# Kernel tuning notes

Hardware: AMD Instinct MI355X
Metric: run time of the kernel (lower is better)

Reference implementation:

```python
import jax, jax.numpy as jnp
import numpy as np


def setup_inputs() -> dict:
    key = jax.random.key(0)
    k1, k2 = jax.random.split(key)
    B, C, H, W = 16, 64, 144, 144
    x = jax.random.normal(k1, (B, C, H, W), dtype=jnp.float32)
    y = jax.random.normal(k2, (B, C, H, W), dtype=jnp.float32)
    return {"x": x, "y": y, "shape": 144}


def reference(x, y, shape):
    # Restrict to the [0:shape, 0:shape] spatial window the Python loop covers.
    xs = x[:, :, :shape, :shape]
    ys = y[:, :, :shape, :shape]
    # Per-pixel reductions over batch AND channel (torch .sum() reduces all
    # remaining dims of x[:, :, i, j], i.e. both B and C).
    fz = jnp.einsum('bchw,bchw->hw', xs, ys)        # [shape, shape]
    xx = jnp.einsum('bchw,bchw->hw', xs, xs)
    yy = jnp.einsum('bchw,bchw->hw', ys, ys)
    fm = jnp.sqrt(xx) * jnp.sqrt(yy)
    loss = jnp.sum(jnp.arccos(fz / fm))
    return loss / (shape ** 2)
```

## Files before the change

### kernel.cpp

```cpp
#include <hip/hip_runtime.h>
#include <math.h>


constexpr int PLANE = 144 * 144;
constexpr int QUADS = PLANE / 4;
constexpr int BC    = 16 * 64;
constexpr int QPB   = 16;
constexpr int NG    = 32;
constexpr int NBLK  = QUADS / QPB;

__device__ inline void xor_fold(float4& v, int mask) {
    v.x += __shfl_xor(v.x, mask);
    v.y += __shfl_xor(v.y, mask);
    v.z += __shfl_xor(v.z, mask);
    v.w += __shfl_xor(v.w, mask);
}

__global__ __launch_bounds__(512) void spe_partial(const float4* __restrict__ x,
                                                   const float4* __restrict__ y,
                                                   float* __restrict__ bsum)
{
    const int tid = threadIdx.x;
    const int q   = tid & (QPB - 1);
    const int g   = tid >> 4;
    const int qg  = blockIdx.x * QPB + q;

    float4 fz = make_float4(0.f, 0.f, 0.f, 0.f);
    float4 xx = make_float4(0.f, 0.f, 0.f, 0.f);
    float4 yy = make_float4(0.f, 0.f, 0.f, 0.f);

    size_t idx = (size_t)g * QUADS + (size_t)qg;
    const size_t step = (size_t)NG * QUADS;
    #pragma unroll 4
    for (int i = 0; i < BC / NG; ++i) {
        float4 a = x[idx];
        float4 b = y[idx];
        fz.x = fmaf(a.x, b.x, fz.x); fz.y = fmaf(a.y, b.y, fz.y);
        fz.z = fmaf(a.z, b.z, fz.z); fz.w = fmaf(a.w, b.w, fz.w);
        xx.x = fmaf(a.x, a.x, xx.x); xx.y = fmaf(a.y, a.y, xx.y);
        xx.z = fmaf(a.z, a.z, xx.z); xx.w = fmaf(a.w, a.w, xx.w);
        yy.x = fmaf(b.x, b.x, yy.x); yy.y = fmaf(b.y, b.y, yy.y);
        yy.z = fmaf(b.z, b.z, yy.z); yy.w = fmaf(b.w, b.w, yy.w);
        idx += step;
    }

    xor_fold(fz, 16); xor_fold(fz, 32);
    xor_fold(xx, 16); xor_fold(xx, 32);
    xor_fold(yy, 16); xor_fold(yy, 32);

    __shared__ float4 lfz[8][QPB], lxx[8][QPB], lyy[8][QPB];
    const int wave = tid >> 6;
    if ((tid & 63) < QPB) {
        lfz[wave][q] = fz; lxx[wave][q] = xx; lyy[wave][q] = yy;
    }
    __syncthreads();

    float s = 0.f;
    if (tid < QPB) {
        float4 F = lfz[0][tid], X = lxx[0][tid], Y = lyy[0][tid];
        #pragma unroll
        for (int wv = 1; wv < 8; ++wv) {
            F.x += lfz[wv][tid].x; F.y += lfz[wv][tid].y;
            F.z += lfz[wv][tid].z; F.w += lfz[wv][tid].w;
            X.x += lxx[wv][tid].x; X.y += lxx[wv][tid].y;
            X.z += lxx[wv][tid].z; X.w += lxx[wv][tid].w;
            Y.x += lyy[wv][tid].x; Y.y += lyy[wv][tid].y;
            Y.z += lyy[wv][tid].z; Y.w += lyy[wv][tid].w;
        }
        float r0 = F.x / (sqrtf(X.x) * sqrtf(Y.x));
        float r1 = F.y / (sqrtf(X.y) * sqrtf(Y.y));
        float r2 = F.z / (sqrtf(X.z) * sqrtf(Y.z));
        float r3 = F.w / (sqrtf(X.w) * sqrtf(Y.w));
        r0 = fminf(1.f, fmaxf(-1.f, r0));
        r1 = fminf(1.f, fmaxf(-1.f, r1));
        r2 = fminf(1.f, fmaxf(-1.f, r2));
        r3 = fminf(1.f, fmaxf(-1.f, r3));
        s = acosf(r0) + acosf(r1) + acosf(r2) + acosf(r3);
    }
    if (tid < 64) {
        #pragma unroll
        for (int off = 32; off >= 1; off >>= 1) s += __shfl_down(s, off);
        if (tid == 0) bsum[blockIdx.x] = s;
    }
}

__global__ __launch_bounds__(512) void spe_final(const float* __restrict__ bsum,
                                                 float* __restrict__ out)
{
    __shared__ float l[8];
    const int t = threadIdx.x;
    float s = (t < NBLK) ? bsum[t] : 0.f;
    #pragma unroll
    for (int off = 32; off >= 1; off >>= 1) s += __shfl_down(s, off);
    if ((t & 63) == 0) l[t >> 6] = s;
    __syncthreads();
    if (t == 0) {
        float tot = 0.f;
        #pragma unroll
        for (int i = 0; i < 8; ++i) tot += l[i];
        out[0] = tot * (1.0f / (float)PLANE);
    }
}

extern "C" void kernel_launch(void* const* d_in, const int* in_sizes, int n_in,
                              void* d_out, int out_size, void* d_ws, size_t ws_size,
                              hipStream_t stream) {
    const float4* x = (const float4*)d_in[0];
    const float4* y = (const float4*)d_in[1];
    float* bsum = (float*)d_ws;
    float* out  = (float*)d_out;

    spe_partial<<<NBLK, 512, 0, stream>>>(x, y, bsum);
    spe_final<<<1, 512, 0, stream>>>(bsum, out);
}
```

Baseline: 35.99 us.

## Split batch-channel reduction across grid y and add a second combine stage

The first kernel previously ran only 324 blocks, each reducing all 1024 batch-channel planes for 64 pixels. The reduction axis is now split eight ways over a second grid dimension (2592 blocks, 4 fully unrolled iterations each), and per-split partial sums are written to workspace. A new stage-2 kernel combines the splits and computes acos per pixel, and a small final kernel sums the block results. The aim is more parallelism and memory-level concurrency on a bandwidth-bound reduction, paid for with an extra launch and roughly 2 MB of partial-sum traffic.

```diff
diff --git a/kernel.cpp b/kernel.cpp
--- a/kernel.cpp
+++ b/kernel.cpp
@@ -7,7 +7,12 @@
 constexpr int BC    = 16 * 64;
 constexpr int QPB   = 16;
 constexpr int NG    = 32;
+constexpr int SPLIT = 8;
+constexpr int BCS   = BC / SPLIT;
+constexpr int ITERS = BCS / NG;
 constexpr int NBLK  = QUADS / QPB;
+constexpr int NPIX  = PLANE;
+constexpr int B2    = 81;
 
 __device__ inline void xor_fold(float4& v, int mask) {
     v.x += __shfl_xor(v.x, mask);
@@ -18,21 +23,24 @@
 
 __global__ __launch_bounds__(512) void spe_partial(const float4* __restrict__ x,
                                                    const float4* __restrict__ y,
-                                                   float* __restrict__ bsum)
+                                                   float4* __restrict__ fzp,
+                                                   float4* __restrict__ xxp,
+                                                   float4* __restrict__ yyp)
 {
     const int tid = threadIdx.x;
     const int q   = tid & (QPB - 1);
     const int g   = tid >> 4;
     const int qg  = blockIdx.x * QPB + q;
+    const int s   = blockIdx.y;
 
     float4 fz = make_float4(0.f, 0.f, 0.f, 0.f);
     float4 xx = make_float4(0.f, 0.f, 0.f, 0.f);
     float4 yy = make_float4(0.f, 0.f, 0.f, 0.f);
 
-    size_t idx = (size_t)g * QUADS + (size_t)qg;
+    size_t idx = ((size_t)s * BCS + g) * QUADS + (size_t)qg;
     const size_t step = (size_t)NG * QUADS;
-    #pragma unroll 4
-    for (int i = 0; i < BC / NG; ++i) {
+    #pragma unroll
+    for (int i = 0; i < ITERS; ++i) {
         float4 a = x[idx];
         float4 b = y[idx];
         fz.x = fmaf(a.x, b.x, fz.x); fz.y = fmaf(a.y, b.y, fz.y);
@@ -55,7 +63,6 @@
     }
     __syncthreads();
 
-    float s = 0.f;
     if (tid < QPB) {
         float4 F = lfz[0][tid], X = lxx[0][tid], Y = lyy[0][tid];
         #pragma unroll
@@ -67,39 +74,49 @@
             Y.x += lyy[wv][tid].x; Y.y += lyy[wv][tid].y;
             Y.z += lyy[wv][tid].z; Y.w += lyy[wv][tid].w;
         }
-        float r0 = F.x / (sqrtf(X.x) * sqrtf(Y.x));
-        float r1 = F.y / (sqrtf(X.y) * sqrtf(Y.y));
-        float r2 = F.z / (sqrtf(X.z) * sqrtf(Y.z));
-        float r3 = F.w / (sqrtf(X.w) * sqrtf(Y.w));
-        r0 = fminf(1.f, fmaxf(-1.f, r0));
-        r1 = fminf(1.f, fmaxf(-1.f, r1));
-        r2 = fminf(1.f, fmaxf(-1.f, r2));
-        r3 = fminf(1.f, fmaxf(-1.f, r3));
-        s = acosf(r0) + acosf(r1) + acosf(r2) + acosf(r3);
-    }
-    if (tid < 64) {
-        #pragma unroll
-        for (int off = 32; off >= 1; off >>= 1) s += __shfl_down(s, off);
-        if (tid == 0) bsum[blockIdx.x] = s;
+        const size_t o = (size_t)s * QUADS + (size_t)(blockIdx.x * QPB + tid);
+        fzp[o] = F; xxp[o] = X; yyp[o] = Y;
     }
 }
 
-__global__ __launch_bounds__(512) void spe_final(const float* __restrict__ bsum,
+__global__ __launch_bounds__(256) void spe_stage2(const float* __restrict__ fzp,
+                                                  const float* __restrict__ xxp,
+                                                  const float* __restrict__ yyp,
+                                                  float* __restrict__ bsum)
+{
+    const int t = threadIdx.x;
+    const int p = blockIdx.x * 256 + t;
+
+    float F = 0.f, X = 0.f, Y = 0.f;
+    #pragma unroll
+    for (int s = 0; s < SPLIT; ++s) {
+        F += fzp[s * NPIX + p];
+        X += xxp[s * NPIX + p];
+        Y += yyp[s * NPIX + p];
+    }
+    float r = F / (sqrtf(X) * sqrtf(Y));
+    r = fminf(1.f, fmaxf(-1.f, r));
+    float v = acosf(r);
+
+    __shared__ float l[4];
+    #pragma unroll
+    for (int off = 32; off >= 1; off >>= 1) v += __shfl_down(v, off);
+    if ((t & 63) == 0) l[t >> 6] = v;
+    __syncthreads();
+    if (t == 0) bsum[blockIdx.x] = l[0] + l[1] + l[2] + l[3];
+}
+
+__global__ __launch_bounds__(128) void spe_final(const float* __restrict__ bsum,
                                                  float* __restrict__ out)
 {
-    __shared__ float l[8];
+    __shared__ float l[2];
     const int t = threadIdx.x;
-    float s = (t < NBLK) ? bsum[t] : 0.f;
+    float s = (t < B2) ? bsum[t] : 0.f;
     #pragma unroll
     for (int off = 32; off >= 1; off >>= 1) s += __shfl_down(s, off);
     if ((t & 63) == 0) l[t >> 6] = s;
     __syncthreads();
-    if (t == 0) {
-        float tot = 0.f;
-        #pragma unroll
-        for (int i = 0; i < 8; ++i) tot += l[i];
-        out[0] = tot * (1.0f / (float)PLANE);
-    }
+    if (t == 0) out[0] = (l[0] + l[1]) * (1.0f / (float)PLANE);
 }
 
 extern "C" void kernel_launch(void* const* d_in, const int* in_sizes, int n_in,
@@ -107,9 +124,16 @@
                               hipStream_t stream) {
     const float4* x = (const float4*)d_in[0];
     const float4* y = (const float4*)d_in[1];
-    float* bsum = (float*)d_ws;
+
+    float* ws  = (float*)d_ws;
+    float* fzp = ws;
+    float* xxp = ws + (size_t)SPLIT * NPIX;
+    float* yyp = ws + (size_t)2 * SPLIT * NPIX;
+    float* bsum = ws + (size_t)3 * SPLIT * NPIX;
     float* out  = (float*)d_out;
 
-    spe_partial<<<NBLK, 512, 0, stream>>>(x, y, bsum);
-    spe_final<<<1, 512, 0, stream>>>(bsum, out);
+    dim3 grid(NBLK, SPLIT);
+    spe_partial<<<grid, 512, 0, stream>>>(x, y, (float4*)fzp, (float4*)xxp, (float4*)yyp);
+    spe_stage2<<<B2, 256, 0, stream>>>(fzp, xxp, yyp, bsum);
+    spe_final<<<1, 128, 0, stream>>>(bsum, out);
 }
```

Result: no change. 35.57 us (-1.2%).
